# Kernel tuning notes

Hardware: AMD Instinct MI355X
Metric: run time of the kernel (lower is better)

Reference implementation:

```python
import jax, jax.numpy as jnp
import numpy as np

N_NODES = 50000
N_EDGES = 600000
D = 128


def setup_inputs() -> dict:
    key = jax.random.key(0)
    k1, k2, k3, k4, k5, k6 = jax.random.split(key, 6)
    x = jax.random.normal(k1, (N_NODES, D), dtype=jnp.float32)
    edge_index = jax.random.randint(k2, (2, N_EDGES), 0, N_NODES, dtype=jnp.int64)
    # nn.Linear default init: U(-1/sqrt(fan_in), 1/sqrt(fan_in))
    bound = 1.0 / np.sqrt(D)
    W1 = jax.random.uniform(k3, (D, D), minval=-bound, maxval=bound, dtype=jnp.float32)
    b1 = jax.random.uniform(k4, (D,), minval=-bound, maxval=bound, dtype=jnp.float32)
    W2 = jax.random.uniform(k5, (D, D), minval=-bound, maxval=bound, dtype=jnp.float32)
    b2 = jax.random.uniform(k6, (D,), minval=-bound, maxval=bound, dtype=jnp.float32)
    return {"x": x, "edge_index": edge_index, "W1": W1, "b1": b1, "W2": W2, "b2": b2}


def reference(x, edge_index, W1, b1, W2, b2):
    row, col = edge_index[0], edge_index[1]
    n = x.shape[0]
    # degree of each node as aggregation target, clamped to >= 1
    deg = jax.ops.segment_sum(jnp.ones(row.shape, dtype=x.dtype), row, num_segments=n)
    deg = jnp.maximum(deg, 1.0)[:, None]  # [N, 1]
    # round 1: gather neighbors, scatter-add by row, normalize, linear+relu
    agg = jax.ops.segment_sum(x[col], row, num_segments=n)  # [N, D]
    h = jax.nn.relu((agg / deg) @ W1.T + b1)
    # round 2
    agg2 = jax.ops.segment_sum(h[col], row, num_segments=n)  # [N, D]
    return jax.nn.relu((agg2 / deg) @ W2.T + b2)
```

## Files before the change

kernel.cpp:

```cpp
#include <hip/hip_runtime.h>
#include <hip/hip_fp16.h>

#define D 128
#define TILE_R 64

typedef _Float16 h8 __attribute__((ext_vector_type(8)));
typedef float f4 __attribute__((ext_vector_type(4)));

__global__ __launch_bounds__(256) void prep_kernel(int* __restrict__ hist, int n,
                                                   const float* __restrict__ W1,
                                                   __half* __restrict__ WB1,
                                                   const float* __restrict__ W2,
                                                   __half* __restrict__ WB2) {
    if (blockIdx.x < 2) {
        const float* W = blockIdx.x ? W2 : W1;
        __half* WB     = blockIdx.x ? WB2 : WB1;
        for (int idx = threadIdx.x; idx < D * D; idx += 256) {
            int j  = idx & 7;
            int l  = (idx >> 3) & 63;
            int kk = (idx >> 9) & 3;
            int c  = idx >> 11;
            int k   = kk * 32 + (l >> 4) * 8 + j;
            int col = c * 16 + (l & 15);
            WB[idx] = __float2half(W[col * D + k]);
        }
        return;
    }
    int i = (blockIdx.x - 2) * 256 + threadIdx.x;
    if (i < n) hist[i] = 0;
}

__global__ __launch_bounds__(256) void hist_kernel(const int* __restrict__ row,
                                                   int* __restrict__ hist, int e) {
    int i = blockIdx.x * blockDim.x + threadIdx.x;
    if (i < e) atomicAdd(&hist[row[i]], 1);
}

__global__ __launch_bounds__(256) void partial_kernel(const int* __restrict__ hist,
                                                      int* __restrict__ bsum, int n) {
    int i = blockIdx.x * 256 + threadIdx.x;
    int v = (i < n) ? hist[i] : 0;
#pragma unroll
    for (int off = 1; off < 64; off <<= 1) v += __shfl_xor(v, off);
    __shared__ int ws[4];
    int lane = threadIdx.x & 63, w = threadIdx.x >> 6;
    if (lane == 0) ws[w] = v;
    __syncthreads();
    if (threadIdx.x == 0) bsum[blockIdx.x] = ws[0] + ws[1] + ws[2] + ws[3];
}

__global__ __launch_bounds__(256) void finalize_kernel(const int* __restrict__ hist,
                                                       const int* __restrict__ bsum,
                                                       int* __restrict__ offsets,
                                                       int* __restrict__ cursor,
                                                       float* __restrict__ rdeg, int n) {
    __shared__ int wt[4];
    int t = threadIdx.x, lane = t & 63, w = t >> 6;

    int p = 0;
    for (int k = t; k < blockIdx.x; k += 256) p += bsum[k];
#pragma unroll
    for (int off = 1; off < 64; off <<= 1) p += __shfl_xor(p, off);
    if (lane == 0) wt[w] = p;
    __syncthreads();
    int blockbase = wt[0] + wt[1] + wt[2] + wt[3];
    __syncthreads();

    int i = blockIdx.x * 256 + t;
    int v = (i < n) ? hist[i] : 0;
    int iv = v;
#pragma unroll
    for (int off = 1; off < 64; off <<= 1) {
        int n2 = __shfl_up(iv, off);
        if (lane >= off) iv += n2;
    }
    if (lane == 63) wt[w] = iv;
    __syncthreads();
    int add = blockbase;
    for (int k = 0; k < w; ++k) add += wt[k];
    int excl = iv - v + add;
    if (i < n) {
        offsets[i] = excl;
        cursor[i]  = excl;
        rdeg[i]    = 1.0f / fmaxf((float)v, 1.0f);
    }
}

__global__ __launch_bounds__(256) void fill_kernel(const int* __restrict__ ei, int e,
                                                   int* __restrict__ cursor,
                                                   int* __restrict__ csr) {
    int i = blockIdx.x * blockDim.x + threadIdx.x;
    if (i < e) {
        int r = ei[i];
        int c = ei[e + i];
        int pos = atomicAdd(&cursor[r], 1);
        csr[pos] = c;
    }
}

__device__ inline h8 load_frag(const __half* p) { return *(const h8*)p; }
__device__ inline h8 load_frag(const float* p) {
    float4 u = *(const float4*)p;
    float4 v = *(const float4*)(p + 4);
    h8 r;
    r[0] = (_Float16)u.x; r[1] = (_Float16)u.y; r[2] = (_Float16)u.z; r[3] = (_Float16)u.w;
    r[4] = (_Float16)v.x; r[5] = (_Float16)v.y; r[6] = (_Float16)v.z; r[7] = (_Float16)v.w;
    return r;
}

template <typename T>
__global__ __launch_bounds__(256) void linear_kernel(const T* __restrict__ src,
                                                     const __half* __restrict__ WB,
                                                     __half* __restrict__ z, int n) {
    alignas(16) __shared__ __half Bs[D * D];
    {
        const float4* wb4 = (const float4*)WB;
        float4* bs4 = (float4*)Bs;
        for (int i = threadIdx.x; i < D * D / 8; i += 256) bs4[i] = wb4[i];
    }
    __syncthreads();

    int l    = threadIdx.x & 63;
    int wv   = threadIdx.x >> 6;
    int row0 = blockIdx.x * TILE_R + wv * 16;
    int arow = row0 + (l & 15);
    bool rowok = arow < n;

    h8 a[4];
#pragma unroll
    for (int kk = 0; kk < 4; ++kk) {
        if (rowok)
            a[kk] = load_frag(&src[(size_t)arow * D + kk * 32 + (l >> 4) * 8]);
        else
            a[kk] = (h8)(_Float16)0.0f;
    }

    int srow = row0 + (l >> 4) * 4;
#pragma unroll
    for (int c = 0; c < 8; ++c) {
        f4 acc = {0.f, 0.f, 0.f, 0.f};
#pragma unroll
        for (int kk = 0; kk < 4; ++kk) {
            h8 b = *(const h8*)&Bs[(((c * 4 + kk) * 64) + l) * 8];
            acc = __builtin_amdgcn_mfma_f32_16x16x32_f16(a[kk], b, acc, 0, 0, 0);
        }
        int col = c * 16 + (l & 15);
#pragma unroll
        for (int r = 0; r < 4; ++r) {
            int ro = srow + r;
            if (ro < n) z[(size_t)ro * D + col] = __float2half(acc[r]);
        }
    }
}

__device__ inline void addh8(float* a, float4 v) {
    const __half2* h = (const __half2*)&v;
    float2 f0 = __half22float2(h[0]);
    float2 f1 = __half22float2(h[1]);
    float2 f2 = __half22float2(h[2]);
    float2 f3 = __half22float2(h[3]);
    a[0] += f0.x; a[1] += f0.y; a[2] += f1.x; a[3] += f1.y;
    a[4] += f2.x; a[5] += f2.y; a[6] += f3.x; a[7] += f3.y;
}

template <int OUT_HALF>
__global__ __launch_bounds__(256) void gather_kernel(const __half* __restrict__ z,
                                                     const int* __restrict__ offsets,
                                                     const int* __restrict__ hist,
                                                     const int* __restrict__ csr,
                                                     const float* __restrict__ rdeg,
                                                     const float* __restrict__ bias,
                                                     void* __restrict__ outv, int n) {
    int tid  = blockIdx.x * 256 + threadIdx.x;
    int wave = tid >> 6;
    int lane = threadIdx.x & 63;
    int g    = lane >> 4;
    int gl   = lane & 15;
    int node = wave * 4 + g;
    if (node >= n) return;

    int start = offsets[node];
    int cnt   = hist[node];
    const float4* base = (const float4*)z;

    float acc[8] = {0.f, 0.f, 0.f, 0.f, 0.f, 0.f, 0.f, 0.f};
    int i = 0;
    for (; i + 8 <= cnt; i += 8) {
        int c0 = csr[start + i];
        int c1 = csr[start + i + 1];
        int c2 = csr[start + i + 2];
        int c3 = csr[start + i + 3];
        int c4 = csr[start + i + 4];
        int c5 = csr[start + i + 5];
        int c6 = csr[start + i + 6];
        int c7 = csr[start + i + 7];
        float4 v0 = base[(size_t)c0 * 16 + gl];
        float4 v1 = base[(size_t)c1 * 16 + gl];
        float4 v2 = base[(size_t)c2 * 16 + gl];
        float4 v3 = base[(size_t)c3 * 16 + gl];
        float4 v4 = base[(size_t)c4 * 16 + gl];
        float4 v5 = base[(size_t)c5 * 16 + gl];
        float4 v6 = base[(size_t)c6 * 16 + gl];
        float4 v7 = base[(size_t)c7 * 16 + gl];
        addh8(acc, v0); addh8(acc, v1); addh8(acc, v2); addh8(acc, v3);
        addh8(acc, v4); addh8(acc, v5); addh8(acc, v6); addh8(acc, v7);
    }
    if (i + 4 <= cnt) {
        int c0 = csr[start + i];
        int c1 = csr[start + i + 1];
        int c2 = csr[start + i + 2];
        int c3 = csr[start + i + 3];
        float4 v0 = base[(size_t)c0 * 16 + gl];
        float4 v1 = base[(size_t)c1 * 16 + gl];
        float4 v2 = base[(size_t)c2 * 16 + gl];
        float4 v3 = base[(size_t)c3 * 16 + gl];
        addh8(acc, v0); addh8(acc, v1); addh8(acc, v2); addh8(acc, v3);
        i += 4;
    }
    int rem = cnt - i;
    if (rem > 0) {
        int c0 = csr[start + i];
        int c1 = csr[start + min(i + 1, cnt - 1)];
        int c2 = csr[start + min(i + 2, cnt - 1)];
        float4 v0 = base[(size_t)c0 * 16 + gl];
        float4 v1 = base[(size_t)c1 * 16 + gl];
        float4 v2 = base[(size_t)c2 * 16 + gl];
        addh8(acc, v0);
        if (rem > 1) addh8(acc, v1);
        if (rem > 2) addh8(acc, v2);
    }

    float rd = rdeg[node];
    float4 b0 = ((const float4*)bias)[gl * 2];
    float4 b1 = ((const float4*)bias)[gl * 2 + 1];
    float o[8];
    o[0] = fmaxf(acc[0] * rd + b0.x, 0.f);
    o[1] = fmaxf(acc[1] * rd + b0.y, 0.f);
    o[2] = fmaxf(acc[2] * rd + b0.z, 0.f);
    o[3] = fmaxf(acc[3] * rd + b0.w, 0.f);
    o[4] = fmaxf(acc[4] * rd + b1.x, 0.f);
    o[5] = fmaxf(acc[5] * rd + b1.y, 0.f);
    o[6] = fmaxf(acc[6] * rd + b1.z, 0.f);
    o[7] = fmaxf(acc[7] * rd + b1.w, 0.f);

    if (OUT_HALF) {
        __half2 h[4];
        h[0] = __float22half2_rn(make_float2(o[0], o[1]));
        h[1] = __float22half2_rn(make_float2(o[2], o[3]));
        h[2] = __float22half2_rn(make_float2(o[4], o[5]));
        h[3] = __float22half2_rn(make_float2(o[6], o[7]));
        ((float4*)outv)[(size_t)node * 16 + gl] = *(const float4*)h;
    } else {
        float4* o4 = (float4*)outv;
        o4[(size_t)node * 32 + gl * 2]     = make_float4(o[0], o[1], o[2], o[3]);
        o4[(size_t)node * 32 + gl * 2 + 1] = make_float4(o[4], o[5], o[6], o[7]);
    }
}

extern "C" void kernel_launch(void* const* d_in, const int* in_sizes, int n_in,
                              void* d_out, int out_size, void* d_ws, size_t ws_size,
                              hipStream_t stream) {
    const float* x  = (const float*)d_in[0];
    const int*   ei = (const int*)d_in[1];
    const float* W1 = (const float*)d_in[2];
    const float* b1 = (const float*)d_in[3];
    const float* W2 = (const float*)d_in[4];
    const float* b2 = (const float*)d_in[5];
    float* out = (float*)d_out;

    int N = in_sizes[0] / D;
    int E = in_sizes[1] / 2;
    int NB = (N + 255) / 256;

    int* hist    = (int*)d_ws;
    int* offsets = hist + N;
    int* cursor  = offsets + N;
    int* csr     = cursor + N;
    float* rdeg  = (float*)(csr + E);
    int* bsum    = (int*)(rdeg + N);
    __half* WB1  = (__half*)(bsum + ((NB + 3) & ~3));
    __half* WB2  = WB1 + D * D;
    __half* hh   = WB2 + D * D;
    __half* zz   = hh + (size_t)N * D;

    prep_kernel<<<NB + 2, 256, 0, stream>>>(hist, N, W1, WB1, W2, WB2);
    hist_kernel<<<(E + 255) / 256, 256, 0, stream>>>(ei, hist, E);
    partial_kernel<<<NB, 256, 0, stream>>>(hist, bsum, N);
    finalize_kernel<<<NB, 256, 0, stream>>>(hist, bsum, offsets, cursor, rdeg, N);
    fill_kernel<<<(E + 255) / 256, 256, 0, stream>>>(ei, E, cursor, csr);

    int nblk = (N + TILE_R - 1) / TILE_R;
    int gblk = ((N + 3) / 4 * 64 + 255) / 256;

    linear_kernel<float><<<nblk, 256, 0, stream>>>(x, WB1, zz, N);
    gather_kernel<1><<<gblk, 256, 0, stream>>>(zz, offsets, hist, csr, rdeg, b1, hh, N);
    linear_kernel<__half><<<nblk, 256, 0, stream>>>(hh, WB2, zz, N);
    gather_kernel<0><<<gblk, 256, 0, stream>>>(zz, offsets, hist, csr, rdeg, b2, out, N);
}
```

Measured before the change: 166.5 us.

## Fuse histogram with first linear and gather-1 with second linear layer

Merges the degree histogram and the first linear projection into one launch by splitting the grid between the two jobs. It also fuses the first gather/normalize/ReLU with the second linear projection, staging each block's 64 aggregated rows in shared memory and running MFMA from there, so the intermediate h no longer round-trips through global memory. Linear layers now read weight fragments straight from global/L2 instead of staging them in LDS. The costs are fewer launches and less intermediate traffic in exchange for 1024-thread blocks in the fused gather, which may hurt occupancy and latency hiding for the irregular gather.

New measurement: 161.6 us. 3.0% less time.

```diff
diff --git a/kernel.cpp b/kernel.cpp
--- a/kernel.cpp
+++ b/kernel.cpp
@@ -30,10 +30,64 @@
     if (i < n) hist[i] = 0;
 }
 
-__global__ __launch_bounds__(256) void hist_kernel(const int* __restrict__ row,
-                                                   int* __restrict__ hist, int e) {
-    int i = blockIdx.x * blockDim.x + threadIdx.x;
-    if (i < e) atomicAdd(&hist[row[i]], 1);
+__device__ inline h8 load_frag(const __half* p) { return *(const h8*)p; }
+__device__ inline h8 load_frag(const float* p) {
+    float4 u = *(const float4*)p;
+    float4 v = *(const float4*)(p + 4);
+    h8 r;
+    r[0] = (_Float16)u.x; r[1] = (_Float16)u.y; r[2] = (_Float16)u.z; r[3] = (_Float16)u.w;
+    r[4] = (_Float16)v.x; r[5] = (_Float16)v.y; r[6] = (_Float16)v.z; r[7] = (_Float16)v.w;
+    return r;
+}
+
+template <typename T>
+__device__ inline void linear_noLDS(const T* __restrict__ src,
+                                    const __half* __restrict__ WB,
+                                    __half* __restrict__ z, int n, int blk) {
+    int l    = threadIdx.x & 63;
+    int wv   = threadIdx.x >> 6;
+    int row0 = blk * TILE_R + wv * 16;
+    int arow = row0 + (l & 15);
+    bool rowok = arow < n;
+
+    h8 a[4];
+#pragma unroll
+    for (int kk = 0; kk < 4; ++kk) {
+        if (rowok)
+            a[kk] = load_frag(&src[(size_t)arow * D + kk * 32 + (l >> 4) * 8]);
+        else
+            a[kk] = (h8)(_Float16)0.0f;
+    }
+
+    int srow = row0 + (l >> 4) * 4;
+#pragma unroll
+    for (int c = 0; c < 8; ++c) {
+        f4 acc = {0.f, 0.f, 0.f, 0.f};
+#pragma unroll
+        for (int kk = 0; kk < 4; ++kk) {
+            h8 b = *(const h8*)&WB[(((c * 4 + kk) * 64) + l) * 8];
+            acc = __builtin_amdgcn_mfma_f32_16x16x32_f16(a[kk], b, acc, 0, 0, 0);
+        }
+        int col = c * 16 + (l & 15);
+#pragma unroll
+        for (int r = 0; r < 4; ++r) {
+            int ro = srow + r;
+            if (ro < n) z[(size_t)ro * D + col] = __float2half(acc[r]);
+        }
+    }
+}
+
+__global__ __launch_bounds__(256) void hist_linear_kernel(const int* __restrict__ ei, int e,
+                                                          int* __restrict__ hist, int nhist,
+                                                          const float* __restrict__ x,
+                                                          const __half* __restrict__ WB,
+                                                          __half* __restrict__ z, int n) {
+    if (blockIdx.x < nhist) {
+        int i = blockIdx.x * 256 + threadIdx.x;
+        if (i < e) atomicAdd(&hist[ei[i]], 1);
+        return;
+    }
+    linear_noLDS<float>(x, WB, z, n, blockIdx.x - nhist);
 }
 
 __global__ __launch_bounds__(256) void partial_kernel(const int* __restrict__ hist,
@@ -98,61 +152,6 @@
     }
 }
 
-__device__ inline h8 load_frag(const __half* p) { return *(const h8*)p; }
-__device__ inline h8 load_frag(const float* p) {
-    float4 u = *(const float4*)p;
-    float4 v = *(const float4*)(p + 4);
-    h8 r;
-    r[0] = (_Float16)u.x; r[1] = (_Float16)u.y; r[2] = (_Float16)u.z; r[3] = (_Float16)u.w;
-    r[4] = (_Float16)v.x; r[5] = (_Float16)v.y; r[6] = (_Float16)v.z; r[7] = (_Float16)v.w;
-    return r;
-}
-
-template <typename T>
-__global__ __launch_bounds__(256) void linear_kernel(const T* __restrict__ src,
-                                                     const __half* __restrict__ WB,
-                                                     __half* __restrict__ z, int n) {
-    alignas(16) __shared__ __half Bs[D * D];
-    {
-        const float4* wb4 = (const float4*)WB;
-        float4* bs4 = (float4*)Bs;
-        for (int i = threadIdx.x; i < D * D / 8; i += 256) bs4[i] = wb4[i];
-    }
-    __syncthreads();
-
-    int l    = threadIdx.x & 63;
-    int wv   = threadIdx.x >> 6;
-    int row0 = blockIdx.x * TILE_R + wv * 16;
-    int arow = row0 + (l & 15);
-    bool rowok = arow < n;
-
-    h8 a[4];
-#pragma unroll
-    for (int kk = 0; kk < 4; ++kk) {
-        if (rowok)
-            a[kk] = load_frag(&src[(size_t)arow * D + kk * 32 + (l >> 4) * 8]);
-        else
-            a[kk] = (h8)(_Float16)0.0f;
-    }
-
-    int srow = row0 + (l >> 4) * 4;
-#pragma unroll
-    for (int c = 0; c < 8; ++c) {
-        f4 acc = {0.f, 0.f, 0.f, 0.f};
-#pragma unroll
-        for (int kk = 0; kk < 4; ++kk) {
-            h8 b = *(const h8*)&Bs[(((c * 4 + kk) * 64) + l) * 8];
-            acc = __builtin_amdgcn_mfma_f32_16x16x32_f16(a[kk], b, acc, 0, 0, 0);
-        }
-        int col = c * 16 + (l & 15);
-#pragma unroll
-        for (int r = 0; r < 4; ++r) {
-            int ro = srow + r;
-            if (ro < n) z[(size_t)ro * D + col] = __float2half(acc[r]);
-        }
-    }
-}
-
 __device__ inline void addh8(float* a, float4 v) {
     const __half2* h = (const __half2*)&v;
     float2 f0 = __half22float2(h[0]);
@@ -163,27 +162,8 @@
     a[4] += f2.x; a[5] += f2.y; a[6] += f3.x; a[7] += f3.y;
 }
 
-template <int OUT_HALF>
-__global__ __launch_bounds__(256) void gather_kernel(const __half* __restrict__ z,
-                                                     const int* __restrict__ offsets,
-                                                     const int* __restrict__ hist,
-                                                     const int* __restrict__ csr,
-                                                     const float* __restrict__ rdeg,
-                                                     const float* __restrict__ bias,
-                                                     void* __restrict__ outv, int n) {
-    int tid  = blockIdx.x * 256 + threadIdx.x;
-    int wave = tid >> 6;
-    int lane = threadIdx.x & 63;
-    int g    = lane >> 4;
-    int gl   = lane & 15;
-    int node = wave * 4 + g;
-    if (node >= n) return;
-
-    int start = offsets[node];
-    int cnt   = hist[node];
-    const float4* base = (const float4*)z;
-
-    float acc[8] = {0.f, 0.f, 0.f, 0.f, 0.f, 0.f, 0.f, 0.f};
+__device__ inline void gather_core(const float4* __restrict__ base, int start, int cnt,
+                                   int gl, const int* __restrict__ csr, float* acc) {
     int i = 0;
     for (; i + 8 <= cnt; i += 8) {
         int c0 = csr[start + i];
@@ -229,32 +209,98 @@
         if (rem > 1) addh8(acc, v1);
         if (rem > 2) addh8(acc, v2);
     }
+}
+
+__global__ __launch_bounds__(1024) void gather_linear_kernel(const __half* __restrict__ z1,
+                                                             const int* __restrict__ offsets,
+                                                             const int* __restrict__ hist,
+                                                             const int* __restrict__ csr,
+                                                             const float* __restrict__ rdeg,
+                                                             const float* __restrict__ bias,
+                                                             const __half* __restrict__ WB2,
+                                                             __half* __restrict__ z2, int n) {
+    __shared__ __half Hs[64][136];
+    int t    = threadIdx.x;
+    int wv   = t >> 6;
+    int lane = t & 63;
+    int g    = lane >> 4;
+    int gl   = lane & 15;
+    int lrow = wv * 4 + g;
+    int node = blockIdx.x * 64 + lrow;
+
+    if (node < n) {
+        float acc[8] = {0.f, 0.f, 0.f, 0.f, 0.f, 0.f, 0.f, 0.f};
+        gather_core((const float4*)z1, offsets[node], hist[node], gl, csr, acc);
+        float rd = rdeg[node];
+        float4 b0 = ((const float4*)bias)[gl * 2];
+        float4 b1 = ((const float4*)bias)[gl * 2 + 1];
+        __half2 hp[4];
+        hp[0] = __float22half2_rn(make_float2(fmaxf(acc[0] * rd + b0.x, 0.f),
+                                              fmaxf(acc[1] * rd + b0.y, 0.f)));
+        hp[1] = __float22half2_rn(make_float2(fmaxf(acc[2] * rd + b0.z, 0.f),
+                                              fmaxf(acc[3] * rd + b0.w, 0.f)));
+        hp[2] = __float22half2_rn(make_float2(fmaxf(acc[4] * rd + b1.x, 0.f),
+                                              fmaxf(acc[5] * rd + b1.y, 0.f)));
+        hp[3] = __float22half2_rn(make_float2(fmaxf(acc[6] * rd + b1.z, 0.f),
+                                              fmaxf(acc[7] * rd + b1.w, 0.f)));
+        *(float4*)&Hs[lrow][gl * 8] = *(const float4*)hp;
+    }
+    __syncthreads();
+
+    int r0 = (wv >> 2) * 16;
+    int arow = r0 + (lane & 15);
+    h8 a[4];
+#pragma unroll
+    for (int kk = 0; kk < 4; ++kk)
+        a[kk] = *(const h8*)&Hs[arow][kk * 32 + (lane >> 4) * 8];
+
+    int srow = blockIdx.x * 64 + r0 + (lane >> 4) * 4;
+#pragma unroll
+    for (int cc = 0; cc < 2; ++cc) {
+        int c = (wv & 3) * 2 + cc;
+        f4 acc = {0.f, 0.f, 0.f, 0.f};
+#pragma unroll
+        for (int kk = 0; kk < 4; ++kk) {
+            h8 b = *(const h8*)&WB2[(((c * 4 + kk) * 64) + lane) * 8];
+            acc = __builtin_amdgcn_mfma_f32_16x16x32_f16(a[kk], b, acc, 0, 0, 0);
+        }
+        int col = c * 16 + (lane & 15);
+#pragma unroll
+        for (int r = 0; r < 4; ++r) {
+            int ro = srow + r;
+            if (ro < n) z2[(size_t)ro * D + col] = __float2half(acc[r]);
+        }
+    }
+}
+
+__global__ __launch_bounds__(256) void gather_kernel(const __half* __restrict__ z,
+                                                     const int* __restrict__ offsets,
+                                                     const int* __restrict__ hist,
+                                                     const int* __restrict__ csr,
+                                                     const float* __restrict__ rdeg,
+                                                     const float* __restrict__ bias,
+                                                     float* __restrict__ out, int n) {
+    int tid  = blockIdx.x * 256 + threadIdx.x;
+    int wave = tid >> 6;
+    int lane = threadIdx.x & 63;
+    int g    = lane >> 4;
+    int gl   = lane & 15;
+    int node = wave * 4 + g;
+    if (node >= n) return;
+
+    float acc[8] = {0.f, 0.f, 0.f, 0.f, 0.f, 0.f, 0.f, 0.f};
+    gather_core((const float4*)z, offsets[node], hist[node], gl, csr, acc);
 
     float rd = rdeg[node];
     float4 b0 = ((const float4*)bias)[gl * 2];
     float4 b1 = ((const float4*)bias)[gl * 2 + 1];
-    float o[8];
-    o[0] = fmaxf(acc[0] * rd + b0.x, 0.f);
-    o[1] = fmaxf(acc[1] * rd + b0.y, 0.f);
-    o[2] = fmaxf(acc[2] * rd + b0.z, 0.f);
-    o[3] = fmaxf(acc[3] * rd + b0.w, 0.f);
-    o[4] = fmaxf(acc[4] * rd + b1.x, 0.f);
-    o[5] = fmaxf(acc[5] * rd + b1.y, 0.f);
-    o[6] = fmaxf(acc[6] * rd + b1.z, 0.f);
-    o[7] = fmaxf(acc[7] * rd + b1.w, 0.f);
-
-    if (OUT_HALF) {
-        __half2 h[4];
-        h[0] = __float22half2_rn(make_float2(o[0], o[1]));
-        h[1] = __float22half2_rn(make_float2(o[2], o[3]));
-        h[2] = __float22half2_rn(make_float2(o[4], o[5]));
-        h[3] = __float22half2_rn(make_float2(o[6], o[7]));
-        ((float4*)outv)[(size_t)node * 16 + gl] = *(const float4*)h;
-    } else {
-        float4* o4 = (float4*)outv;
-        o4[(size_t)node * 32 + gl * 2]     = make_float4(o[0], o[1], o[2], o[3]);
-        o4[(size_t)node * 32 + gl * 2 + 1] = make_float4(o[4], o[5], o[6], o[7]);
-    }
+    float4* o4 = (float4*)out;
+    o4[(size_t)node * 32 + gl * 2] =
+        make_float4(fmaxf(acc[0] * rd + b0.x, 0.f), fmaxf(acc[1] * rd + b0.y, 0.f),
+                    fmaxf(acc[2] * rd + b0.z, 0.f), fmaxf(acc[3] * rd + b0.w, 0.f));
+    o4[(size_t)node * 32 + gl * 2 + 1] =
+        make_float4(fmaxf(acc[4] * rd + b1.x, 0.f), fmaxf(acc[5] * rd + b1.y, 0.f),
+                    fmaxf(acc[6] * rd + b1.z, 0.f), fmaxf(acc[7] * rd + b1.w, 0.f));
 }
 
 extern "C" void kernel_launch(void* const* d_in, const int* in_sizes, int n_in,
@@ -280,20 +326,19 @@
     int* bsum    = (int*)(rdeg + N);
     __half* WB1  = (__half*)(bsum + ((NB + 3) & ~3));
     __half* WB2  = WB1 + D * D;
-    __half* hh   = WB2 + D * D;
-    __half* zz   = hh + (size_t)N * D;
+    __half* zz   = WB2 + D * D;
+    __half* zz2  = zz + (size_t)N * D;
+
+    int nhist = (E + 255) / 256;
+    int nblk  = (N + TILE_R - 1) / TILE_R;
+    int gblk  = ((N + 3) / 4 * 64 + 255) / 256;
 
     prep_kernel<<<NB + 2, 256, 0, stream>>>(hist, N, W1, WB1, W2, WB2);
-    hist_kernel<<<(E + 255) / 256, 256, 0, stream>>>(ei, hist, E);
+    hist_linear_kernel<<<nhist + nblk, 256, 0, stream>>>(ei, E, hist, nhist, x, WB1, zz, N);
     partial_kernel<<<NB, 256, 0, stream>>>(hist, bsum, N);
     finalize_kernel<<<NB, 256, 0, stream>>>(hist, bsum, offsets, cursor, rdeg, N);
     fill_kernel<<<(E + 255) / 256, 256, 0, stream>>>(ei, E, cursor, csr);
-
-    int nblk = (N + TILE_R - 1) / TILE_R;
-    int gblk = ((N + 3) / 4 * 64 + 255) / 256;
-
-    linear_kernel<float><<<nblk, 256, 0, stream>>>(x, WB1, zz, N);
-    gather_kernel<1><<<gblk, 256, 0, stream>>>(zz, offsets, hist, csr, rdeg, b1, hh, N);
-    linear_kernel<__half><<<nblk, 256, 0, stream>>>(hh, WB2, zz, N);
-    gather_kernel<0><<<gblk, 256, 0, stream>>>(zz, offsets, hist, csr, rdeg, b2, out, N);
-}
+    gather_linear_kernel<<<nblk, 1024, 0, stream>>>(zz, offsets, hist, csr, rdeg, b1,
+                                                    WB2, zz2, N);
+    gather_kernel<<<gblk, 256, 0, stream>>>(zz2, offsets, hist, csr, rdeg, b2, out, N);
+}
```
